# Kernel optimization log

Measured on AMD Instinct MI355X. Metric: run time of the kernel, lower is better.

The kernel has to match this reference:

```python
import jax, jax.numpy as jnp
import numpy as np

N_NODES = 50000
N_EDGES = 800000
IN_FEATS = 128
OUT_FEATS = 128


def setup_inputs() -> dict:
    key = jax.random.key(0)
    k1, k2, k3, k4, k5 = jax.random.split(key, 5)
    feature = jax.random.normal(k1, (N_NODES, IN_FEATS), dtype=jnp.float32)
    src_idx = jax.random.randint(k2, (N_EDGES,), 0, N_NODES, dtype=jnp.int32)
    dst_idx = jax.random.randint(k3, (N_EDGES,), 0, N_NODES, dtype=jnp.int32)
    # nn.Linear(in, out): weight [out, in], bias [out]
    bound = 1.0 / np.sqrt(IN_FEATS)
    W = jax.random.uniform(k4, (OUT_FEATS, IN_FEATS), minval=-bound, maxval=bound, dtype=jnp.float32)
    b = jax.random.uniform(k5, (OUT_FEATS,), minval=-bound, maxval=bound, dtype=jnp.float32)
    return {"feature": feature, "src_idx": src_idx, "dst_idx": dst_idx, "W": W, "b": b}


def reference(feature, src_idx, dst_idx, W, b):
    # message: copy src node feature along each edge; reduce: sum into dst node
    msgs = feature[src_idx]                                   # [E, F_in] gather
    agg = jax.ops.segment_sum(msgs, dst_idx, num_segments=N_NODES)  # [N, F_in]
    # apply: linear + relu
    h = jax.nn.relu(agg @ W.T + b)                            # [N, F_out]
    return h
```

## Files before the change

kernel.cpp:

```cpp
#include <hip/hip_runtime.h>
#include <hip/hip_fp16.h>

#define F 128
#define TILE 256
#define TSH 8
#define CHUNK 4096
#define BCAP 8192
#define ROWS2 32
#define LINB 256
#define SCAN_TILE 1024

typedef _Float16 f16x8 __attribute__((ext_vector_type(8)));
typedef float f32x4 __attribute__((ext_vector_type(4)));

__device__ inline float4 h8_to_f4(uint2 u) {
    union { unsigned int x; __half2 h; } a, b;
    a.x = u.x; b.x = u.y;
    const float2 lo = __half22float2(a.h);
    const float2 hi = __half22float2(b.h);
    return make_float4(lo.x, lo.y, hi.x, hi.y);
}

__global__ __launch_bounds__(256) void prep_count_kernel(
        const float* __restrict__ feat, unsigned int* __restrict__ featH,
        const float* __restrict__ W, __half* __restrict__ woh,
        int* __restrict__ offsets, const int* __restrict__ dst,
        int* __restrict__ blkCnt,
        int N, int NF4, int E, int NT, int NCHUNK) {
    __shared__ int h[256];
    const int tid = threadIdx.x;
    const int bid = blockIdx.x;
    if (bid < NCHUNK) {
        h[tid] = 0;
        __syncthreads();
        const int e0 = bid * CHUNK;
        const int n = min(CHUNK, E - e0);
        for (int i = tid; i < n; i += 256) atomicAdd(&h[dst[e0 + i] >> TSH], 1);
        __syncthreads();
        if (tid < NT) blkCnt[(size_t)tid * NCHUNK + bid] = h[tid];
    } else {
        const int i = (bid - NCHUNK) * 256 + tid;
        if (i < NF4) {
            const float4 v = ((const float4*)feat)[i];
            union { __half2 h2; unsigned int u; } a, b;
            a.h2 = __floats2half2_rn(v.x, v.y);
            b.h2 = __floats2half2_rn(v.z, v.w);
            ((uint2*)featH)[i] = make_uint2(a.u, b.u);
        }
        if (i < F * F) woh[i] = __float2half(W[i]);
        if (i == 0 && (N & (TILE - 1)) == 0) offsets[N] = 0;
    }
}

__global__ __launch_bounds__(256) void binA_scan_kernel(
        const int* __restrict__ blkCnt, int* __restrict__ blkOff,
        int* __restrict__ bucketBase, int E, int NT, int NCHUNK) {
    __shared__ int red[256];
    const int t = blockIdx.x;
    const int tid = threadIdx.x;

    const int lim = t * NCHUNK;
    int s = 0;
    for (int i = tid; i < lim; i += 256) s += blkCnt[i];
    red[tid] = s;
    __syncthreads();
    for (int off = 128; off > 0; off >>= 1) {
        if (tid < off) red[tid] += red[tid + off];
        __syncthreads();
    }
    const int base = red[0];
    __syncthreads();

    int carry = base;
    for (int c0 = 0; c0 < NCHUNK; c0 += 256) {
        const int b = c0 + tid;
        const int v = (b < NCHUNK) ? blkCnt[(size_t)t * NCHUNK + b] : 0;
        red[tid] = v;
        __syncthreads();
        for (int off = 1; off < 256; off <<= 1) {
            int tv = (tid >= off) ? red[tid - off] : 0;
            __syncthreads();
            red[tid] += tv;
            __syncthreads();
        }
        const int excl = red[tid] - v;
        if (b < NCHUNK) blkOff[(size_t)t * NCHUNK + b] = carry + excl;
        const int tot = red[255];
        __syncthreads();
        carry += tot;
    }
    if (tid == 0) {
        bucketBase[t] = base;
        if (t == 0) bucketBase[NT] = E;
    }
}

__global__ __launch_bounds__(256) void binA_scatter_kernel(
        const int* __restrict__ src, const int* __restrict__ dst,
        const int* __restrict__ blkOff,
        unsigned int* __restrict__ edgebuf, int E, int NT, int NCHUNK) {
    __shared__ int h[256];
    __shared__ int lds2[256];
    __shared__ int cstart[256];
    __shared__ uint2 stage[CHUNK];
    const int tid = threadIdx.x, b = blockIdx.x;
    h[tid] = 0;
    __syncthreads();
    const int e0 = b * CHUNK;
    const int n = min(CHUNK, E - e0);
    for (int i = tid; i < n; i += 256) atomicAdd(&h[dst[e0 + i] >> TSH], 1);
    __syncthreads();
    const int myc = h[tid];
    lds2[tid] = myc;
    __syncthreads();
    for (int off = 1; off < 256; off <<= 1) {
        int t = (tid >= off) ? lds2[tid - off] : 0;
        __syncthreads();
        lds2[tid] += t;
        __syncthreads();
    }
    const int runstart = lds2[tid] - myc;
    if (tid < NT) cstart[tid] = blkOff[(size_t)tid * NCHUNK + b] - runstart;
    h[tid] = runstart;
    __syncthreads();
    for (int i = tid; i < n; i += 256) {
        const int e = e0 + i;
        const int d = dst[e];
        const int p = atomicAdd(&h[d >> TSH], 1);
        stage[p] = make_uint2((unsigned)src[e], (unsigned)d);
    }
    __syncthreads();
    for (int i = tid; i < n; i += 256) {
        const uint2 v = stage[i];
        const int t = (int)v.y >> TSH;
        edgebuf[cstart[t] + i] = (v.x << 8) | (v.y & 255u);
    }
}

__global__ __launch_bounds__(256) void build_tile_kernel(
        const unsigned int* __restrict__ edgebuf, const int* __restrict__ bucketBase,
        int* __restrict__ offsets, int* __restrict__ ssrc, int N, int NT) {
    __shared__ int h[TILE];
    __shared__ int excl[TILE];
    __shared__ int stage[BCAP];
    const int t = blockIdx.x, tid = threadIdx.x;
    const int s0 = bucketBase[t], s1 = bucketBase[t + 1];
    const int cnt = s1 - s0;
    const int n0 = t << TSH;
    const int n1 = min(n0 + TILE, N);
    h[tid] = 0;
    __syncthreads();
    for (int i = tid; i < cnt; i += 256)
        atomicAdd(&h[(int)(edgebuf[s0 + i] & 255u)], 1);
    __syncthreads();
    const int myv = h[tid];
    excl[tid] = myv;
    __syncthreads();
    for (int off = 1; off < 256; off <<= 1) {
        int tv = (tid >= off) ? excl[tid - off] : 0;
        __syncthreads();
        excl[tid] += tv;
        __syncthreads();
    }
    const int ex = excl[tid] - myv;
    const int v = n0 + tid;
    if (v < n1) offsets[v] = ex;
    if (tid == 255 && n1 == N && (N & (TILE - 1)) != 0) offsets[N] = excl[255];
    h[tid] = ex;
    __syncthreads();
    if (cnt <= BCAP) {
        for (int i = tid; i < cnt; i += 256) {
            const unsigned int e = edgebuf[s0 + i];
            const int p = atomicAdd(&h[(int)(e & 255u)], 1);
            stage[p] = (int)(e >> 8);
        }
        __syncthreads();
        for (int i = tid; i < cnt; i += 256) ssrc[s0 + i] = stage[i];
    } else {
        for (int i = tid; i < cnt; i += 256) {
            const unsigned int e = edgebuf[s0 + i];
            const int p = atomicAdd(&h[(int)(e & 255u)], 1);
            ssrc[s0 + p] = (int)(e >> 8);
        }
    }
}

__global__ __launch_bounds__(256) void agg16_kernel(
        const uint4* __restrict__ fH,
        const int* __restrict__ ssrc,
        const int* __restrict__ offs,
        const int* __restrict__ base,
        uint4* __restrict__ aggH, int N) {
    const int gwave = (blockIdx.x * blockDim.x + threadIdx.x) >> 6;
    const int lane = threadIdx.x & 63;
    const int g = lane >> 4;
    const int q = lane & 15;
    const int nwaves = (gridDim.x * blockDim.x) >> 6;

    for (int v = gwave; v < N; v += nwaves) {
        const int s0 = offs[v] + base[v >> TSH];
        const int s1 = offs[v + 1] + base[(v + 1) >> TSH];
        float a[8];
#pragma unroll
        for (int j = 0; j < 8; ++j) a[j] = 0.f;

        int e = s0 + g;
        for (; e + 4 < s1; e += 8) {
            const int i0 = ssrc[e], i1 = ssrc[e + 4];
            const uint4 u0 = fH[(size_t)i0 * 16 + q];
            const uint4 u1 = fH[(size_t)i1 * 16 + q];
            {
                union { unsigned int u; __half2 h; } c0, c1, c2, c3;
                c0.u = u0.x; c1.u = u0.y; c2.u = u0.z; c3.u = u0.w;
                const float2 f0 = __half22float2(c0.h);
                const float2 f1 = __half22float2(c1.h);
                const float2 f2 = __half22float2(c2.h);
                const float2 f3 = __half22float2(c3.h);
                a[0] += f0.x; a[1] += f0.y; a[2] += f1.x; a[3] += f1.y;
                a[4] += f2.x; a[5] += f2.y; a[6] += f3.x; a[7] += f3.y;
            }
            {
                union { unsigned int u; __half2 h; } c0, c1, c2, c3;
                c0.u = u1.x; c1.u = u1.y; c2.u = u1.z; c3.u = u1.w;
                const float2 f0 = __half22float2(c0.h);
                const float2 f1 = __half22float2(c1.h);
                const float2 f2 = __half22float2(c2.h);
                const float2 f3 = __half22float2(c3.h);
                a[0] += f0.x; a[1] += f0.y; a[2] += f1.x; a[3] += f1.y;
                a[4] += f2.x; a[5] += f2.y; a[6] += f3.x; a[7] += f3.y;
            }
        }
        for (; e < s1; e += 4) {
            const uint4 u0 = fH[(size_t)ssrc[e] * 16 + q];
            union { unsigned int u; __half2 h; } c0, c1, c2, c3;
            c0.u = u0.x; c1.u = u0.y; c2.u = u0.z; c3.u = u0.w;
            const float2 f0 = __half22float2(c0.h);
            const float2 f1 = __half22float2(c1.h);
            const float2 f2 = __half22float2(c2.h);
            const float2 f3 = __half22float2(c3.h);
            a[0] += f0.x; a[1] += f0.y; a[2] += f1.x; a[3] += f1.y;
            a[4] += f2.x; a[5] += f2.y; a[6] += f3.x; a[7] += f3.y;
        }

#pragma unroll
        for (int j = 0; j < 8; ++j) {
            a[j] += __shfl_xor(a[j], 16);
            a[j] += __shfl_xor(a[j], 32);
        }
        if (g == 0) {
            union { __half2 h2; unsigned int u; } p0, p1, p2, p3;
            p0.h2 = __floats2half2_rn(a[0], a[1]);
            p1.h2 = __floats2half2_rn(a[2], a[3]);
            p2.h2 = __floats2half2_rn(a[4], a[5]);
            p3.h2 = __floats2half2_rn(a[6], a[7]);
            aggH[(size_t)v * 16 + q] = make_uint4(p0.u, p1.u, p2.u, p3.u);
        }
    }
}

__global__ __launch_bounds__(256) void linear_mfma_kernel(
        const uint4* __restrict__ aggH,
        const uint4* __restrict__ woh4,
        const float* __restrict__ bias,
        float* __restrict__ out, int N) {
    const int tid = threadIdx.x;
    const int wid = tid >> 6;
    const int lane = tid & 63;
    const int m16 = lane & 15;
    const int kq = lane >> 4;
    const int row0 = blockIdx.x * 64 + wid * 16;
    const int rowA = row0 + m16;

    union U { uint4 u; f16x8 h; };
    U af[4];
    if (rowA < N) {
        const uint4* r = aggH + (size_t)rowA * 16 + kq;
        af[0].u = r[0]; af[1].u = r[4]; af[2].u = r[8]; af[3].u = r[12];
    } else {
        af[0].u = af[1].u = af[2].u = af[3].u = make_uint4(0u, 0u, 0u, 0u);
    }

#pragma unroll
    for (int g = 0; g < 8; ++g) {
        const uint4* wrow = woh4 + (size_t)(g * 16 + m16) * 16 + kq;
        U b0, b1, b2, b3;
        b0.u = wrow[0]; b1.u = wrow[4]; b2.u = wrow[8]; b3.u = wrow[12];
        f32x4 acc = {0.f, 0.f, 0.f, 0.f};
        acc = __builtin_amdgcn_mfma_f32_16x16x32_f16(af[0].h, b0.h, acc, 0, 0, 0);
        acc = __builtin_amdgcn_mfma_f32_16x16x32_f16(af[1].h, b1.h, acc, 0, 0, 0);
        acc = __builtin_amdgcn_mfma_f32_16x16x32_f16(af[2].h, b2.h, acc, 0, 0, 0);
        acc = __builtin_amdgcn_mfma_f32_16x16x32_f16(af[3].h, b3.h, acc, 0, 0, 0);
        const float bv = bias[g * 16 + m16];
#pragma unroll
        for (int r = 0; r < 4; ++r) {
            const int gr = row0 + kq * 4 + r;
            if (gr < N)
                out[(size_t)gr * F + g * 16 + m16] = fmaxf(acc[r] + bv, 0.f);
        }
    }
}

__global__ void prep2_kernel(const float* __restrict__ W, __half* __restrict__ wTh,
                             int* __restrict__ counts, int N) {
    int i = blockIdx.x * 256 + threadIdx.x;
    if (i < F * F) {
        int o = i >> 7, k = i & 127;
        wTh[k * F + o] = __float2half(W[i]);
    }
    if (i < N) counts[i] = 0;
}

__global__ void hist_kernel(const int* __restrict__ dst, int* __restrict__ counts, int E) {
    int e = blockIdx.x * blockDim.x + threadIdx.x;
    if (e < E) atomicAdd(&counts[dst[e]], 1);
}

__global__ __launch_bounds__(256) void scan1_kernel(const int* __restrict__ counts,
                                                    int* __restrict__ offsets,
                                                    int* __restrict__ cursor,
                                                    int* __restrict__ blockSums, int N) {
    __shared__ int lds[256];
    const int tid = threadIdx.x;
    const int i0 = blockIdx.x * SCAN_TILE + tid * 4;
    int v[4];
    int s = 0;
#pragma unroll
    for (int j = 0; j < 4; ++j) {
        int i = i0 + j;
        v[j] = (i < N) ? counts[i] : 0;
        s += v[j];
    }
    lds[tid] = s;
    __syncthreads();
    for (int off = 1; off < 256; off <<= 1) {
        int t = (tid >= off) ? lds[tid - off] : 0;
        __syncthreads();
        lds[tid] += t;
        __syncthreads();
    }
    int excl = lds[tid] - s;
#pragma unroll
    for (int j = 0; j < 4; ++j) {
        int i = i0 + j;
        if (i < N) {
            offsets[i] = excl;
            cursor[i] = excl;
        } else if (i == N) {
            offsets[N] = excl;
        }
        excl += v[j];
    }
    if (tid == 255) blockSums[blockIdx.x] = lds[255];
}

__global__ __launch_bounds__(256) void scan2_kernel(int* __restrict__ blockSums,
                                                    int* __restrict__ offsets,
                                                    int NB, int N) {
    __shared__ int lds[256];
    const int tid = threadIdx.x;
    int s = (tid < NB) ? blockSums[tid] : 0;
    lds[tid] = s;
    __syncthreads();
    for (int off = 1; off < 256; off <<= 1) {
        int t = (tid >= off) ? lds[tid - off] : 0;
        __syncthreads();
        lds[tid] += t;
        __syncthreads();
    }
    if (tid < NB) blockSums[tid] = lds[tid] - s;
    if (tid == NB && NB < 256) blockSums[NB] = lds[255];
    if (tid == 0 && (N & (SCAN_TILE - 1)) == 0) offsets[N] = 0;
}

__global__ void place_kernel(const int* __restrict__ src, const int* __restrict__ dst,
                             int* __restrict__ cursor, const int* __restrict__ base,
                             int* __restrict__ ssrc, int E) {
    int e = blockIdx.x * blockDim.x + threadIdx.x;
    if (e < E) {
        int d = dst[e];
        int pos = atomicAdd(&cursor[d], 1) + base[d >> 10];
        ssrc[pos] = src[e];
    }
}

__global__ __launch_bounds__(256) void agg_kernel(const float* __restrict__ feat,
                                                  const int* __restrict__ ssrc,
                                                  const int* __restrict__ offs,
                                                  const int* __restrict__ base,
                                                  float* __restrict__ out, int N) {
    const int gwave = (blockIdx.x * blockDim.x + threadIdx.x) >> 6;
    const int lane = threadIdx.x & 63;
    const int half = lane >> 5;
    const int q = lane & 31;
    const int nwaves = (gridDim.x * blockDim.x) >> 6;
    const float4* feat4 = (const float4*)feat;
    for (int v = gwave; v < N; v += nwaves) {
        const int s0 = offs[v] + base[v >> 10];
        const int s1 = offs[v + 1] + base[(v + 1) >> 10];
        float ax = 0.f, ay = 0.f, az = 0.f, aw = 0.f;
        int e = s0 + half;
        for (; e + 6 < s1; e += 8) {
            int i0 = ssrc[e], i1 = ssrc[e + 2], i2 = ssrc[e + 4], i3 = ssrc[e + 6];
            const float4 f0 = feat4[(size_t)i0 * 32 + q];
            const float4 f1 = feat4[(size_t)i1 * 32 + q];
            const float4 f2 = feat4[(size_t)i2 * 32 + q];
            const float4 f3 = feat4[(size_t)i3 * 32 + q];
            ax += (f0.x + f1.x) + (f2.x + f3.x);
            ay += (f0.y + f1.y) + (f2.y + f3.y);
            az += (f0.z + f1.z) + (f2.z + f3.z);
            aw += (f0.w + f1.w) + (f2.w + f3.w);
        }
        for (; e < s1; e += 2) {
            const float4 f0 = feat4[(size_t)ssrc[e] * 32 + q];
            ax += f0.x; ay += f0.y; az += f0.z; aw += f0.w;
        }
        ax += __shfl_xor(ax, 32);
        ay += __shfl_xor(ay, 32);
        az += __shfl_xor(az, 32);
        aw += __shfl_xor(aw, 32);
        if (half == 0) {
            float4 r;
            r.x = ax; r.y = ay; r.z = az; r.w = aw;
            ((float4*)(out + (size_t)v * F))[q] = r;
        }
    }
}

__global__ __launch_bounds__(LINB) void linear_relu_kernel(
        float* __restrict__ h, const __half* __restrict__ wTh,
        const float* __restrict__ b, int N) {
    __shared__ __align__(16) float sA[ROWS2][132];
    const int tid = threadIdx.x;
    const int row0 = blockIdx.x * ROWS2;

    for (int i = tid; i < ROWS2 * 32; i += LINB) {
        int r = i >> 5, q = i & 31;
        int gr = row0 + r;
        float4 v = make_float4(0.f, 0.f, 0.f, 0.f);
        if (gr < N) v = ((const float4*)(h + (size_t)gr * F))[q];
        *((float4*)&sA[r][q << 2]) = v;
    }
    __syncthreads();

    const int tr = tid >> 5;
    const int tc = tid & 31;
    float acc[4][4];
#pragma unroll
    for (int i = 0; i < 4; ++i)
#pragma unroll
        for (int j = 0; j < 4; ++j) acc[i][j] = 0.f;

    const uint2* wTh2 = (const uint2*)wTh;
    uint2 u0 = wTh2[0 * 32 + tc];
    uint2 u1 = wTh2[1 * 32 + tc];
    uint2 u2 = wTh2[2 * 32 + tc];
    uint2 u3 = wTh2[3 * 32 + tc];

#pragma unroll 1
    for (int k = 0; k < F - 4; k += 4) {
        const uint2 p0 = wTh2[(k + 4) * 32 + tc];
        const uint2 p1 = wTh2[(k + 5) * 32 + tc];
        const uint2 p2 = wTh2[(k + 6) * 32 + tc];
        const uint2 p3 = wTh2[(k + 7) * 32 + tc];
        const float4 w0 = h8_to_f4(u0);
        const float4 w1 = h8_to_f4(u1);
        const float4 w2 = h8_to_f4(u2);
        const float4 w3 = h8_to_f4(u3);
#pragma unroll
        for (int i = 0; i < 4; ++i) {
            const float4 a = *(const float4*)&sA[tr * 4 + i][k];
            acc[i][0] += a.x * w0.x + a.y * w1.x + a.z * w2.x + a.w * w3.x;
            acc[i][1] += a.x * w0.y + a.y * w1.y + a.z * w2.y + a.w * w3.y;
            acc[i][2] += a.x * w0.z + a.y * w1.z + a.z * w2.z + a.w * w3.z;
            acc[i][3] += a.x * w0.w + a.y * w1.w + a.z * w2.w + a.w * w3.w;
        }
        u0 = p0; u1 = p1; u2 = p2; u3 = p3;
    }
    {
        const int k = F - 4;
        const float4 w0 = h8_to_f4(u0);
        const float4 w1 = h8_to_f4(u1);
        const float4 w2 = h8_to_f4(u2);
        const float4 w3 = h8_to_f4(u3);
#pragma unroll
        for (int i = 0; i < 4; ++i) {
            const float4 a = *(const float4*)&sA[tr * 4 + i][k];
            acc[i][0] += a.x * w0.x + a.y * w1.x + a.z * w2.x + a.w * w3.x;
            acc[i][1] += a.x * w0.y + a.y * w1.y + a.z * w2.y + a.w * w3.y;
            acc[i][2] += a.x * w0.z + a.y * w1.z + a.z * w2.z + a.w * w3.z;
            acc[i][3] += a.x * w0.w + a.y * w1.w + a.z * w2.w + a.w * w3.w;
        }
    }

    const float4 bias = ((const float4*)b)[tc];
#pragma unroll
    for (int i = 0; i < 4; ++i) {
        int gr = row0 + tr * 4 + i;
        if (gr < N) {
            float4 o;
            o.x = fmaxf(acc[i][0] + bias.x, 0.f);
            o.y = fmaxf(acc[i][1] + bias.y, 0.f);
            o.z = fmaxf(acc[i][2] + bias.z, 0.f);
            o.w = fmaxf(acc[i][3] + bias.w, 0.f);
            ((float4*)(h + (size_t)gr * F))[tc] = o;
        }
    }
}

__global__ void zero_f4_kernel(float4* __restrict__ out, int n4) {
    int i = blockIdx.x * blockDim.x + threadIdx.x;
    if (i < n4) out[i] = make_float4(0.f, 0.f, 0.f, 0.f);
}

__global__ void scatter_atomic_kernel(const float* __restrict__ feat,
                                      const int* __restrict__ src,
                                      const int* __restrict__ dst,
                                      float* __restrict__ agg, int E) {
    int gid = blockIdx.x * blockDim.x + threadIdx.x;
    int e = gid >> 5;
    if (e >= E) return;
    int q = gid & 31;
    int s = src[e];
    int d = dst[e];
    const float4 v = ((const float4*)(feat + (size_t)s * F))[q];
    float* o = agg + (size_t)d * F + (q << 2);
    atomicAdd(o + 0, v.x);
    atomicAdd(o + 1, v.y);
    atomicAdd(o + 2, v.z);
    atomicAdd(o + 3, v.w);
}

__global__ __launch_bounds__(256) void linear_relu_w_kernel(
        float* __restrict__ h, const float* __restrict__ W,
        const float* __restrict__ b, int N) {
    __shared__ __align__(16) float sA[64][132];
    const int tid = threadIdx.x;
    const int row0 = blockIdx.x * 64;

    for (int i = tid; i < 64 * 32; i += 256) {
        int r = i >> 5, q = i & 31;
        int gr = row0 + r;
        float4 v = make_float4(0.f, 0.f, 0.f, 0.f);
        if (gr < N) v = ((const float4*)(h + (size_t)gr * F))[q];
        *((float4*)&sA[r][q << 2]) = v;
    }
    __syncthreads();

    const int tr = tid >> 5;
    const int tc = tid & 31;
    float acc[8][4];
#pragma unroll
    for (int i = 0; i < 8; ++i)
#pragma unroll
        for (int j = 0; j < 4; ++j) acc[i][j] = 0.f;

    const float* Wr0 = W + (size_t)(tc * 4 + 0) * F;
    const float* Wr1 = W + (size_t)(tc * 4 + 1) * F;
    const float* Wr2 = W + (size_t)(tc * 4 + 2) * F;
    const float* Wr3 = W + (size_t)(tc * 4 + 3) * F;

    for (int k = 0; k < F; k += 4) {
        const float4 w0 = *(const float4*)&Wr0[k];
        const float4 w1 = *(const float4*)&Wr1[k];
        const float4 w2 = *(const float4*)&Wr2[k];
        const float4 w3 = *(const float4*)&Wr3[k];
#pragma unroll
        for (int i = 0; i < 8; ++i) {
            const float4 a = *(const float4*)&sA[tr * 8 + i][k];
            acc[i][0] += a.x * w0.x + a.y * w0.y + a.z * w0.z + a.w * w0.w;
            acc[i][1] += a.x * w1.x + a.y * w1.y + a.z * w1.z + a.w * w1.w;
            acc[i][2] += a.x * w2.x + a.y * w2.y + a.z * w2.z + a.w * w2.w;
            acc[i][3] += a.x * w3.x + a.y * w3.y + a.z * w3.z + a.w * w3.w;
        }
    }

    const float4 bias = ((const float4*)b)[tc];
#pragma unroll
    for (int i = 0; i < 8; ++i) {
        int gr = row0 + tr * 8 + i;
        if (gr < N) {
            float4 o;
            o.x = fmaxf(acc[i][0] + bias.x, 0.f);
            o.y = fmaxf(acc[i][1] + bias.y, 0.f);
            o.z = fmaxf(acc[i][2] + bias.z, 0.f);
            o.w = fmaxf(acc[i][3] + bias.w, 0.f);
            ((float4*)(h + (size_t)gr * F))[tc] = o;
        }
    }
}

extern "C" void kernel_launch(void* const* d_in, const int* in_sizes, int n_in,
                              void* d_out, int out_size, void* d_ws, size_t ws_size,
                              hipStream_t stream) {
    const float* feat = (const float*)d_in[0];
    const int*   src  = (const int*)d_in[1];
    const int*   dst  = (const int*)d_in[2];
    const float* W    = (const float*)d_in[3];
    const float* b    = (const float*)d_in[4];
    float* out = (float*)d_out;

    const int N = in_sizes[0] / F;
    const int E = in_sizes[1];
    const int NT = (N + TILE - 1) / TILE;
    const int NCHUNK = (E + CHUNK - 1) / CHUNK;
    const int NB = (N + SCAN_TILE - 1) / SCAN_TILE;

    auto align4 = [](size_t x) { return (x + 3) & ~(size_t)3; };

    const size_t o_featH = 0;
    const size_t o_aggH  = align4(o_featH + (size_t)N * 64);
    const size_t o_woh   = align4(o_aggH + (size_t)N * 64);
    const size_t o_offs  = align4(o_woh + (size_t)(F * F) / 2);
    const size_t o_bb    = align4(o_offs + (size_t)N + 1);
    const size_t o_blk   = align4(o_bb + (size_t)NT + 1);
    const size_t o_boff  = align4(o_blk + (size_t)NT * NCHUNK);
    const size_t o_ebuf  = align4(o_boff + (size_t)NT * NCHUNK);
    const size_t o_ssrc  = align4(o_ebuf + (size_t)E);
    const size_t need_main = (o_ssrc + (size_t)E) * sizeof(int);

    const size_t csr_ints = (size_t)(F * F) / 2 + N + (N + 1) + N + 260 + E;
    const size_t need_mid = csr_ints * sizeof(int);
    const bool nb_ok = (NB < 256) || ((N & (SCAN_TILE - 1)) != 0 && NB <= 256);

    if (ws_size >= need_main && NT <= 256 && N < (1 << 24)) {
        unsigned int* featH = (unsigned int*)d_ws;
        uint4* aggH          = (uint4*)((int*)d_ws + o_aggH);
        __half* woh          = (__half*)((int*)d_ws + o_woh);
        int* offsets         = (int*)d_ws + o_offs;
        int* bucketBase      = (int*)d_ws + o_bb;
        int* blkCnt          = (int*)d_ws + o_blk;
        int* blkOff          = (int*)d_ws + o_boff;
        unsigned int* edgebuf = (unsigned int*)((int*)d_ws + o_ebuf);
        int* ssrc            = (int*)d_ws + o_ssrc;

        const int NF4 = N * 32;
        const int nprep = (NF4 + 255) / 256;
        prep_count_kernel<<<NCHUNK + nprep, 256, 0, stream>>>(
            feat, featH, W, woh, offsets, dst, blkCnt, N, NF4, E, NT, NCHUNK);
        binA_scan_kernel<<<NT, 256, 0, stream>>>(blkCnt, blkOff, bucketBase, E, NT, NCHUNK);
        binA_scatter_kernel<<<NCHUNK, 256, 0, stream>>>(src, dst, blkOff, edgebuf, E, NT, NCHUNK);
        build_tile_kernel<<<NT, 256, 0, stream>>>(edgebuf, bucketBase, offsets, ssrc, N, NT);
        agg16_kernel<<<2048, 256, 0, stream>>>((const uint4*)featH, ssrc, offsets, bucketBase, aggH, N);
        linear_mfma_kernel<<<(N + 63) / 64, 256, 0, stream>>>(
            (const uint4*)aggH, (const uint4*)woh, b, out, N);
    } else if (ws_size >= need_mid && nb_ok) {
        __half* wTh    = (__half*)d_ws;
        int* counts    = (int*)d_ws + (F * F) / 2;
        int* offsets   = counts + N;
        int* cursor    = offsets + (N + 1);
        int* blockSums = cursor + N;
        int* ssrc      = blockSums + 260;

        prep2_kernel<<<(N + 255) / 256, 256, 0, stream>>>(W, wTh, counts, N);
        hist_kernel<<<(E + 255) / 256, 256, 0, stream>>>(dst, counts, E);
        scan1_kernel<<<NB, 256, 0, stream>>>(counts, offsets, cursor, blockSums, N);
        scan2_kernel<<<1, 256, 0, stream>>>(blockSums, offsets, NB, N);
        place_kernel<<<(E + 255) / 256, 256, 0, stream>>>(src, dst, cursor, blockSums, ssrc, E);
        agg_kernel<<<2048, 256, 0, stream>>>(feat, ssrc, offsets, blockSums, out, N);
        linear_relu_kernel<<<(N + ROWS2 - 1) / ROWS2, LINB, 0, stream>>>(out, wTh, b, N);
    } else {
        const int n4 = N * (F / 4);
        zero_f4_kernel<<<(n4 + 255) / 256, 256, 0, stream>>>((float4*)out, n4);
        const int sthreads = E * 32;
        scatter_atomic_kernel<<<(sthreads + 255) / 256, 256, 0, stream>>>(feat, src, dst, out, E);
        linear_relu_w_kernel<<<(N + 63) / 64, 256, 0, stream>>>(out, W, b, N);
    }
}
```

Measured before the change: 180.3 us.

## Fuse neighbor aggregation with MFMA linear layer via per-wave LDS tile

Merges the gather-sum aggregation and the fp16 MFMA linear+ReLU into a single kernel. Each wave aggregates 16 destination nodes into a padded LDS buffer, then loads A fragments from LDS and runs the MFMA. This removes the global aggH intermediate write/read and one kernel launch. The trade-off is fewer waves in flight (one per 16 nodes), which reduces latency hiding for the random gathers.

```diff
diff --git a/kernel.cpp b/kernel.cpp
--- a/kernel.cpp
+++ b/kernel.cpp
@@ -185,117 +185,115 @@
     }
 }
 
-__global__ __launch_bounds__(256) void agg16_kernel(
+__global__ __launch_bounds__(256) void agg_mfma_kernel(
         const uint4* __restrict__ fH,
         const int* __restrict__ ssrc,
         const int* __restrict__ offs,
         const int* __restrict__ base,
-        uint4* __restrict__ aggH, int N) {
-    const int gwave = (blockIdx.x * blockDim.x + threadIdx.x) >> 6;
-    const int lane = threadIdx.x & 63;
-    const int g = lane >> 4;
-    const int q = lane & 15;
-    const int nwaves = (gridDim.x * blockDim.x) >> 6;
-
-    for (int v = gwave; v < N; v += nwaves) {
-        const int s0 = offs[v] + base[v >> TSH];
-        const int s1 = offs[v + 1] + base[(v + 1) >> TSH];
-        float a[8];
-#pragma unroll
-        for (int j = 0; j < 8; ++j) a[j] = 0.f;
-
-        int e = s0 + g;
-        for (; e + 4 < s1; e += 8) {
-            const int i0 = ssrc[e], i1 = ssrc[e + 4];
-            const uint4 u0 = fH[(size_t)i0 * 16 + q];
-            const uint4 u1 = fH[(size_t)i1 * 16 + q];
-            {
-                union { unsigned int u; __half2 h; } c0, c1, c2, c3;
-                c0.u = u0.x; c1.u = u0.y; c2.u = u0.z; c3.u = u0.w;
-                const float2 f0 = __half22float2(c0.h);
-                const float2 f1 = __half22float2(c1.h);
-                const float2 f2 = __half22float2(c2.h);
-                const float2 f3 = __half22float2(c3.h);
-                a[0] += f0.x; a[1] += f0.y; a[2] += f1.x; a[3] += f1.y;
-                a[4] += f2.x; a[5] += f2.y; a[6] += f3.x; a[7] += f3.y;
-            }
-            {
-                union { unsigned int u; __half2 h; } c0, c1, c2, c3;
-                c0.u = u1.x; c1.u = u1.y; c2.u = u1.z; c3.u = u1.w;
-                const float2 f0 = __half22float2(c0.h);
-                const float2 f1 = __half22float2(c1.h);
-                const float2 f2 = __half22float2(c2.h);
-                const float2 f3 = __half22float2(c3.h);
-                a[0] += f0.x; a[1] += f0.y; a[2] += f1.x; a[3] += f1.y;
-                a[4] += f2.x; a[5] += f2.y; a[6] += f3.x; a[7] += f3.y;
-            }
-        }
-        for (; e < s1; e += 4) {
-            const uint4 u0 = fH[(size_t)ssrc[e] * 16 + q];
-            union { unsigned int u; __half2 h; } c0, c1, c2, c3;
-            c0.u = u0.x; c1.u = u0.y; c2.u = u0.z; c3.u = u0.w;
-            const float2 f0 = __half22float2(c0.h);
-            const float2 f1 = __half22float2(c1.h);
-            const float2 f2 = __half22float2(c2.h);
-            const float2 f3 = __half22float2(c3.h);
-            a[0] += f0.x; a[1] += f0.y; a[2] += f1.x; a[3] += f1.y;
-            a[4] += f2.x; a[5] += f2.y; a[6] += f3.x; a[7] += f3.y;
-        }
-
-#pragma unroll
-        for (int j = 0; j < 8; ++j) {
-            a[j] += __shfl_xor(a[j], 16);
-            a[j] += __shfl_xor(a[j], 32);
-        }
-        if (g == 0) {
-            union { __half2 h2; unsigned int u; } p0, p1, p2, p3;
-            p0.h2 = __floats2half2_rn(a[0], a[1]);
-            p1.h2 = __floats2half2_rn(a[2], a[3]);
-            p2.h2 = __floats2half2_rn(a[4], a[5]);
-            p3.h2 = __floats2half2_rn(a[6], a[7]);
-            aggH[(size_t)v * 16 + q] = make_uint4(p0.u, p1.u, p2.u, p3.u);
-        }
-    }
-}
-
-__global__ __launch_bounds__(256) void linear_mfma_kernel(
-        const uint4* __restrict__ aggH,
         const uint4* __restrict__ woh4,
         const float* __restrict__ bias,
         float* __restrict__ out, int N) {
+    __shared__ __align__(16) uint4 abuf[4][16 * 17];
     const int tid = threadIdx.x;
     const int wid = tid >> 6;
     const int lane = tid & 63;
-    const int m16 = lane & 15;
-    const int kq = lane >> 4;
-    const int row0 = blockIdx.x * 64 + wid * 16;
-    const int rowA = row0 + m16;
-
-    union U { uint4 u; f16x8 h; };
-    U af[4];
-    if (rowA < N) {
-        const uint4* r = aggH + (size_t)rowA * 16 + kq;
-        af[0].u = r[0]; af[1].u = r[4]; af[2].u = r[8]; af[3].u = r[12];
-    } else {
-        af[0].u = af[1].u = af[2].u = af[3].u = make_uint4(0u, 0u, 0u, 0u);
-    }
-
-#pragma unroll
-    for (int g = 0; g < 8; ++g) {
-        const uint4* wrow = woh4 + (size_t)(g * 16 + m16) * 16 + kq;
-        U b0, b1, b2, b3;
-        b0.u = wrow[0]; b1.u = wrow[4]; b2.u = wrow[8]; b3.u = wrow[12];
-        f32x4 acc = {0.f, 0.f, 0.f, 0.f};
-        acc = __builtin_amdgcn_mfma_f32_16x16x32_f16(af[0].h, b0.h, acc, 0, 0, 0);
-        acc = __builtin_amdgcn_mfma_f32_16x16x32_f16(af[1].h, b1.h, acc, 0, 0, 0);
-        acc = __builtin_amdgcn_mfma_f32_16x16x32_f16(af[2].h, b2.h, acc, 0, 0, 0);
-        acc = __builtin_amdgcn_mfma_f32_16x16x32_f16(af[3].h, b3.h, acc, 0, 0, 0);
-        const float bv = bias[g * 16 + m16];
-#pragma unroll
-        for (int r = 0; r < 4; ++r) {
-            const int gr = row0 + kq * 4 + r;
-            if (gr < N)
-                out[(size_t)gr * F + g * 16 + m16] = fmaxf(acc[r] + bv, 0.f);
+    const int g = lane >> 4;
+    const int q = lane & 15;
+    const int gwave = (blockIdx.x * blockDim.x + tid) >> 6;
+    const int nwaves = (gridDim.x * blockDim.x) >> 6;
+    const int ntiles = (N + 15) >> 4;
+    uint4* buf = abuf[wid];
+
+    for (int tile = gwave; tile < ntiles; tile += nwaves) {
+        const int v0 = tile << 4;
+
+        for (int t = 0; t < 16; ++t) {
+            const int v = v0 + t;
+            float a[8];
+#pragma unroll
+            for (int j = 0; j < 8; ++j) a[j] = 0.f;
+            if (v < N) {
+                const int s0 = offs[v] + base[v >> TSH];
+                const int s1 = offs[v + 1] + base[(v + 1) >> TSH];
+                int e = s0 + g;
+                for (; e + 4 < s1; e += 8) {
+                    const int i0 = ssrc[e], i1 = ssrc[e + 4];
+                    const uint4 u0 = fH[(size_t)i0 * 16 + q];
+                    const uint4 u1 = fH[(size_t)i1 * 16 + q];
+                    {
+                        union { unsigned int u; __half2 h; } c0, c1, c2, c3;
+                        c0.u = u0.x; c1.u = u0.y; c2.u = u0.z; c3.u = u0.w;
+                        const float2 f0 = __half22float2(c0.h);
+                        const float2 f1 = __half22float2(c1.h);
+                        const float2 f2 = __half22float2(c2.h);
+                        const float2 f3 = __half22float2(c3.h);
+                        a[0] += f0.x; a[1] += f0.y; a[2] += f1.x; a[3] += f1.y;
+                        a[4] += f2.x; a[5] += f2.y; a[6] += f3.x; a[7] += f3.y;
+                    }
+                    {
+                        union { unsigned int u; __half2 h; } c0, c1, c2, c3;
+                        c0.u = u1.x; c1.u = u1.y; c2.u = u1.z; c3.u = u1.w;
+                        const float2 f0 = __half22float2(c0.h);
+                        const float2 f1 = __half22float2(c1.h);
+                        const float2 f2 = __half22float2(c2.h);
+                        const float2 f3 = __half22float2(c3.h);
+                        a[0] += f0.x; a[1] += f0.y; a[2] += f1.x; a[3] += f1.y;
+                        a[4] += f2.x; a[5] += f2.y; a[6] += f3.x; a[7] += f3.y;
+                    }
+                }
+                for (; e < s1; e += 4) {
+                    const uint4 u0 = fH[(size_t)ssrc[e] * 16 + q];
+                    union { unsigned int u; __half2 h; } c0, c1, c2, c3;
+                    c0.u = u0.x; c1.u = u0.y; c2.u = u0.z; c3.u = u0.w;
+                    const float2 f0 = __half22float2(c0.h);
+                    const float2 f1 = __half22float2(c1.h);
+                    const float2 f2 = __half22float2(c2.h);
+                    const float2 f3 = __half22float2(c3.h);
+                    a[0] += f0.x; a[1] += f0.y; a[2] += f1.x; a[3] += f1.y;
+                    a[4] += f2.x; a[5] += f2.y; a[6] += f3.x; a[7] += f3.y;
+                }
+            }
+#pragma unroll
+            for (int j = 0; j < 8; ++j) {
+                a[j] += __shfl_xor(a[j], 16);
+                a[j] += __shfl_xor(a[j], 32);
+            }
+            if (g == 0) {
+                union { __half2 h2; unsigned int u; } p0, p1, p2, p3;
+                p0.h2 = __floats2half2_rn(a[0], a[1]);
+                p1.h2 = __floats2half2_rn(a[2], a[3]);
+                p2.h2 = __floats2half2_rn(a[4], a[5]);
+                p3.h2 = __floats2half2_rn(a[6], a[7]);
+                buf[t * 17 + q] = make_uint4(p0.u, p1.u, p2.u, p3.u);
+            }
+        }
+        asm volatile("s_waitcnt lgkmcnt(0)" ::: "memory");
+        __builtin_amdgcn_sched_barrier(0);
+
+        union U { uint4 u; f16x8 h; };
+        U af0, af1, af2, af3;
+        af0.u = buf[q * 17 + (g + 0)];
+        af1.u = buf[q * 17 + (g + 4)];
+        af2.u = buf[q * 17 + (g + 8)];
+        af3.u = buf[q * 17 + (g + 12)];
+
+#pragma unroll
+        for (int gg = 0; gg < 8; ++gg) {
+            const uint4* wrow = woh4 + (size_t)(gg * 16 + q) * 16 + g;
+            U b0, b1, b2, b3;
+            b0.u = wrow[0]; b1.u = wrow[4]; b2.u = wrow[8]; b3.u = wrow[12];
+            f32x4 acc = {0.f, 0.f, 0.f, 0.f};
+            acc = __builtin_amdgcn_mfma_f32_16x16x32_f16(af0.h, b0.h, acc, 0, 0, 0);
+            acc = __builtin_amdgcn_mfma_f32_16x16x32_f16(af1.h, b1.h, acc, 0, 0, 0);
+            acc = __builtin_amdgcn_mfma_f32_16x16x32_f16(af2.h, b2.h, acc, 0, 0, 0);
+            acc = __builtin_amdgcn_mfma_f32_16x16x32_f16(af3.h, b3.h, acc, 0, 0, 0);
+            const float bv = bias[gg * 16 + q];
+#pragma unroll
+            for (int r = 0; r < 4; ++r) {
+                const int gr = v0 + g * 4 + r;
+                if (gr < N)
+                    out[(size_t)gr * F + gg * 16 + q] = fmaxf(acc[r] + bv, 0.f);
+            }
         }
     }
 }
@@ -608,8 +606,7 @@
     auto align4 = [](size_t x) { return (x + 3) & ~(size_t)3; };
 
     const size_t o_featH = 0;
-    const size_t o_aggH  = align4(o_featH + (size_t)N * 64);
-    const size_t o_woh   = align4(o_aggH + (size_t)N * 64);
+    const size_t o_woh   = align4(o_featH + (size_t)N * 64);
     const size_t o_offs  = align4(o_woh + (size_t)(F * F) / 2);
     const size_t o_bb    = align4(o_offs + (size_t)N + 1);
     const size_t o_blk   = align4(o_bb + (size_t)NT + 1);
@@ -624,7 +621,6 @@
 
     if (ws_size >= need_main && NT <= 256 && N < (1 << 24)) {
         unsigned int* featH = (unsigned int*)d_ws;
-        uint4* aggH          = (uint4*)((int*)d_ws + o_aggH);
         __half* woh          = (__half*)((int*)d_ws + o_woh);
         int* offsets         = (int*)d_ws + o_offs;
         int* bucketBase      = (int*)d_ws + o_bb;
@@ -640,9 +636,11 @@
         binA_scan_kernel<<<NT, 256, 0, stream>>>(blkCnt, blkOff, bucketBase, E, NT, NCHUNK);
         binA_scatter_kernel<<<NCHUNK, 256, 0, stream>>>(src, dst, blkOff, edgebuf, E, NT, NCHUNK);
         build_tile_kernel<<<NT, 256, 0, stream>>>(edgebuf, bucketBase, offsets, ssrc, N, NT);
-        agg16_kernel<<<2048, 256, 0, stream>>>((const uint4*)featH, ssrc, offsets, bucketBase, aggH, N);
-        linear_mfma_kernel<<<(N + 63) / 64, 256, 0, stream>>>(
-            (const uint4*)aggH, (const uint4*)woh, b, out, N);
+        const int ntiles = (N + 15) / 16;
+        const int ablocks = (ntiles + 3) / 4;
+        agg_mfma_kernel<<<ablocks, 256, 0, stream>>>(
+            (const uint4*)featH, ssrc, offsets, bucketBase,
+            (const uint4*)woh, b, out, N);
     } else if (ws_size >= need_mid && nb_ok) {
         __half* wTh    = (__half*)d_ws;
         int* counts    = (int*)d_ws + (F * F) / 2;
```

New measurement: 188.1 us. +4.3%, slower.
